# Kernel tuning notes

Measured on AMD Instinct MI355X. Metric: run time of the kernel, lower is better.

Reference implementation:

```python
import jax, jax.numpy as jnp
import numpy as np

D_MODEL = 1024
N_HEAD = 16
D_K = D_MODEL // N_HEAD
B, S = 2, 2048


def setup_inputs() -> dict:
    key = jax.random.key(0)
    ks = jax.random.split(key, 13)
    sc = 0.02
    return {
        "q": jax.random.normal(ks[0], (B, S, D_MODEL), jnp.float32),
        "k": jax.random.normal(ks[1], (B, S, D_MODEL), jnp.float32),
        "v": jax.random.normal(ks[2], (B, S, D_MODEL), jnp.float32),
        "mask": jax.random.randint(ks[3], (B, 1, S, S), 0, 2, jnp.int32),
        "Wq": jax.random.normal(ks[4], (D_MODEL, D_MODEL), jnp.float32) * sc,
        "bq": jnp.zeros((D_MODEL,), jnp.float32),
        "Wk": jax.random.normal(ks[5], (D_MODEL, D_MODEL), jnp.float32) * sc,
        "bk": jnp.zeros((D_MODEL,), jnp.float32),
        "Wv": jax.random.normal(ks[6], (D_MODEL, D_MODEL), jnp.float32) * sc,
        "bv": jnp.zeros((D_MODEL,), jnp.float32),
        "Wo": jax.random.normal(ks[7], (D_MODEL, D_MODEL), jnp.float32) * sc,
        "bo": jnp.zeros((D_MODEL,), jnp.float32),
    }


def _split_head(x):
    # (B, S, D) -> (B, H, S, d_k)
    b, s, _ = x.shape
    return x.reshape(b, s, N_HEAD, D_K).transpose(0, 2, 1, 3)


def reference(q, k, v, mask, Wq, bq, Wk, bk, Wv, bv, Wo, bo):
    qh = _split_head(q @ Wq.T + bq)
    kh = _split_head(k @ Wk.T + bk)
    vh = _split_head(v @ Wv.T + bv)
    # NOTE: original scales by sqrt(d_model), not sqrt(d_k)
    score = jnp.einsum("bhqd,bhkd->bhqk", qh, kh) / jnp.sqrt(jnp.float32(D_MODEL))
    score = jnp.where(mask == 0, jnp.float32(-1e9), score)
    attn = jax.nn.softmax(score, axis=-1)
    out = jnp.einsum("bhqk,bhkd->bhqd", attn, vh)
    out = out.transpose(0, 2, 1, 3).reshape(q.shape[0], -1, D_MODEL)
    return out @ Wo.T + bo
```

## Files before the change

kernel.cpp:

```cpp
#include <hip/hip_runtime.h>

#define D_MODEL 1024
#define N_HEAD  16
#define D_K     64
#define BATCH   2
#define SEQ     2048
#define M_ROWS  (BATCH*SEQ)
#define NT      (SEQ/64)

typedef __attribute__((ext_vector_type(8))) short short8;
typedef __attribute__((ext_vector_type(4))) float f32x4;
typedef unsigned short u16;
typedef unsigned long long u64;

#define GLDS16(g, l) \
    __builtin_amdgcn_global_load_lds((const __attribute__((address_space(1))) void*)(g), \
                                     (__attribute__((address_space(3))) void*)(l), 16, 0, 0)

#define CSC (0.03125f * 1.44269504089f)

__device__ __forceinline__ u16 f2bf(float f) {
    unsigned u = __builtin_bit_cast(unsigned, f);
    unsigned r = (u + 0x7fffu + ((u >> 16) & 1u)) >> 16;
    return (u16)r;
}

__device__ __forceinline__ float fexp2(float x) {
#if __has_builtin(__builtin_amdgcn_exp2f)
    return __builtin_amdgcn_exp2f(x);
#else
    return exp2f(x);
#endif
}

__global__ __launch_bounds__(256)
void cvt_all(const float* __restrict__ q, const float* __restrict__ k, const float* __restrict__ v,
             const float* __restrict__ wq, const float* __restrict__ wk,
             const float* __restrict__ wv, const float* __restrict__ wo,
             u16* __restrict__ qb, u16* __restrict__ kb, u16* __restrict__ vb,
             u16* __restrict__ wqb, u16* __restrict__ wkb, u16* __restrict__ wvb, u16* __restrict__ wob)
{
    const int total = 3 * 1048576 + 4 * 262144;
    int i = blockIdx.x * blockDim.x + threadIdx.x;
    const int stride = gridDim.x * blockDim.x;
    for (; i < total; i += stride) {
        const float* src; u16* dst; int loc;
        if (i < 3 * 1048576) {
            const int t = i >> 20; loc = i & 1048575;
            src = (t == 0) ? q : (t == 1) ? k : v;
            dst = (t == 0) ? qb : (t == 1) ? kb : vb;
        } else {
            const int j = i - 3 * 1048576; const int t = j >> 18; loc = j & 262143;
            src = (t == 0) ? wq : (t == 1) ? wk : (t == 2) ? wv : wo;
            dst = (t == 0) ? wqb : (t == 1) ? wkb : (t == 2) ? wvb : wob;
        }
        float4 a = ((const float4*)src)[loc];
        ushort4 o;
        o.x = f2bf(a.x); o.y = f2bf(a.y); o.z = f2bf(a.z); o.w = f2bf(a.w);
        ((ushort4*)dst)[loc] = o;
    }
}

__global__ __launch_bounds__(256)
void mask_pack(const int* __restrict__ mask, u64* __restrict__ mb, int nwords)
{
    const int lane = threadIdx.x & 63;
    int w = (blockIdx.x * blockDim.x + threadIdx.x) >> 6;
    const int nw = (gridDim.x * blockDim.x) >> 6;
    for (; w < nwords; w += nw) {
        int v = mask[(size_t)w * 64 + lane];
        u64 bits = __ballot(v != 0);
        if (lane == 0) mb[w] = bits;
    }
}

template<bool OUT_BF16, bool BIAS_ROW, bool SCALE>
__device__ __forceinline__
void gemm128_body(const u16* __restrict__ A, const u16* __restrict__ W,
                  const float* __restrict__ bias, void* __restrict__ Cout,
                  const int M, const int N, const int K, const int bx, const int by)
{
    __shared__ u16 As[2][128 * 32];
    __shared__ u16 Ws[2][128 * 32];
    const int tid = threadIdx.x, l = tid & 63, w = tid >> 6;
    const int bm = by * 128, bn = bx * 128;
    const int wr = (w >> 1) * 64, wc = (w & 1) * 64;
    const int srow = tid >> 2, scol = (tid & 3) * 8;
    const u16* Ap = A + (size_t)(bm + srow) * K + scol;
    const u16* Wp = W + (size_t)(bn + srow) * K + scol;

    f32x4 acc[4][4];
#pragma unroll
    for (int m = 0; m < 4; ++m)
#pragma unroll
        for (int n = 0; n < 4; ++n) acc[m][n] = (f32x4)0.0f;

    const int ro = l & 15, ge = (l >> 4) * 8;

    GLDS16(Ap,                  (char*)As[0] + w * 1024);
    GLDS16(Ap + (size_t)64 * K, (char*)As[0] + w * 1024 + 4096);
    GLDS16(Wp,                  (char*)Ws[0] + w * 1024);
    GLDS16(Wp + (size_t)64 * K, (char*)Ws[0] + w * 1024 + 4096);
    __syncthreads();

    int buf = 0;
    for (int k0 = 0; k0 < K; k0 += 32) {
        if (k0 + 32 < K) {
            GLDS16(Ap + k0 + 32,                  (char*)As[buf ^ 1] + w * 1024);
            GLDS16(Ap + k0 + 32 + (size_t)64 * K, (char*)As[buf ^ 1] + w * 1024 + 4096);
            GLDS16(Wp + k0 + 32,                  (char*)Ws[buf ^ 1] + w * 1024);
            GLDS16(Wp + k0 + 32 + (size_t)64 * K, (char*)Ws[buf ^ 1] + w * 1024 + 4096);
        }
        short8 a[4], b[4];
#pragma unroll
        for (int m = 0; m < 4; ++m)
            a[m] = *(const short8*)(As[buf] + (wr + m * 16 + ro) * 32 + ge);
#pragma unroll
        for (int n = 0; n < 4; ++n)
            b[n] = *(const short8*)(Ws[buf] + (wc + n * 16 + ro) * 32 + ge);
#pragma unroll
        for (int m = 0; m < 4; ++m)
#pragma unroll
            for (int n = 0; n < 4; ++n)
                acc[m][n] = __builtin_amdgcn_mfma_f32_16x16x32_bf16(a[m], b[n], acc[m][n], 0, 0, 0);
        __syncthreads();
        buf ^= 1;
    }

    const int cr = (l >> 4) * 4;
#pragma unroll
    for (int m = 0; m < 4; ++m)
#pragma unroll
        for (int n = 0; n < 4; ++n)
#pragma unroll
            for (int j = 0; j < 4; ++j) {
                const int row = bm + wr + m * 16 + cr + j;
                const int col = bn + wc + n * 16 + ro;
                float vvv = acc[m][n][j] + (BIAS_ROW ? bias[row] : bias[col]);
                if constexpr (SCALE) vvv *= CSC;
                if constexpr (OUT_BF16)
                    ((u16*)Cout)[(size_t)row * N + col] = f2bf(vvv);
                else
                    ((float*)Cout)[(size_t)row * N + col] = vvv;
            }
}

__global__ __launch_bounds__(256)
void gemm_proj(const u16* __restrict__ qb, const u16* __restrict__ kb, const u16* __restrict__ vb,
               const u16* __restrict__ wqb, const u16* __restrict__ wkb, const u16* __restrict__ wvb,
               const float* __restrict__ bq, const float* __restrict__ bk, const float* __restrict__ bv,
               u16* __restrict__ Qp, u16* __restrict__ Kp, u16* __restrict__ Vt)
{
    int lin = blockIdx.x;
    lin = (lin & 7) * 32 + (lin >> 3);
    const int z = blockIdx.y;
    if (z == 0)
        gemm128_body<true, false, true >(qb, wqb, bq, Qp, M_ROWS, D_MODEL, D_MODEL, lin & 7, lin >> 3);
    else if (z == 1)
        gemm128_body<true, false, false>(kb, wkb, bk, Kp, M_ROWS, D_MODEL, D_MODEL, lin & 7, lin >> 3);
    else
        gemm128_body<true, true,  false>(wvb, vb, bv, Vt, D_MODEL, M_ROWS, D_MODEL, lin & 31, lin >> 5);
}

__device__ __forceinline__
void gemm64_body(const u16* __restrict__ A, const u16* __restrict__ W,
                 const float* __restrict__ bias, float* __restrict__ Cout,
                 const int N, const int K, const int bx, const int by)
{
    __shared__ u16 As[2][128 * 32];
    __shared__ u16 Ws[2][64 * 32];
    const int tid = threadIdx.x, l = tid & 63, w = tid >> 6;
    const int bm = by * 128, bn = bx * 64;
    const int wr = (w >> 1) * 64, wc = (w & 1) * 32;
    const int srow = tid >> 2, scol = (tid & 3) * 8;
    const u16* Ap = A + (size_t)(bm + srow) * K + scol;
    const u16* Wp = W + (size_t)(bn + srow) * K + scol;

    f32x4 acc[4][2];
#pragma unroll
    for (int m = 0; m < 4; ++m)
#pragma unroll
        for (int n = 0; n < 2; ++n) acc[m][n] = (f32x4)0.0f;

    const int ro = l & 15, ge = (l >> 4) * 8;

    GLDS16(Ap,                  (char*)As[0] + w * 1024);
    GLDS16(Ap + (size_t)64 * K, (char*)As[0] + w * 1024 + 4096);
    GLDS16(Wp,                  (char*)Ws[0] + w * 1024);
    __syncthreads();

    int buf = 0;
    for (int k0 = 0; k0 < K; k0 += 32) {
        if (k0 + 32 < K) {
            GLDS16(Ap + k0 + 32,                  (char*)As[buf ^ 1] + w * 1024);
            GLDS16(Ap + k0 + 32 + (size_t)64 * K, (char*)As[buf ^ 1] + w * 1024 + 4096);
            GLDS16(Wp + k0 + 32,                  (char*)Ws[buf ^ 1] + w * 1024);
        }
        short8 a[4], b[2];
#pragma unroll
        for (int m = 0; m < 4; ++m)
            a[m] = *(const short8*)(As[buf] + (wr + m * 16 + ro) * 32 + ge);
#pragma unroll
        for (int n = 0; n < 2; ++n)
            b[n] = *(const short8*)(Ws[buf] + (wc + n * 16 + ro) * 32 + ge);
#pragma unroll
        for (int m = 0; m < 4; ++m)
#pragma unroll
            for (int n = 0; n < 2; ++n)
                acc[m][n] = __builtin_amdgcn_mfma_f32_16x16x32_bf16(a[m], b[n], acc[m][n], 0, 0, 0);
        __syncthreads();
        buf ^= 1;
    }

    const int cr = (l >> 4) * 4;
#pragma unroll
    for (int m = 0; m < 4; ++m)
#pragma unroll
        for (int n = 0; n < 2; ++n)
#pragma unroll
            for (int j = 0; j < 4; ++j) {
                const int row = bm + wr + m * 16 + cr + j;
                const int col = bn + wc + n * 16 + ro;
                Cout[(size_t)row * N + col] = acc[m][n][j] + bias[col];
            }
}

__global__ __launch_bounds__(256)
void gemm_out(const u16* __restrict__ Ctx, const u16* __restrict__ wob,
              const float* __restrict__ bo, float* __restrict__ out)
{
    int lin = blockIdx.y * gridDim.x + blockIdx.x;
    const int cpx = (gridDim.x * gridDim.y) >> 3;
    lin = (lin & 7) * cpx + (lin >> 3);
    const int bx = lin % gridDim.x, by = lin / gridDim.x;
    gemm64_body(Ctx, wob, bo, out, D_MODEL, D_MODEL, bx, by);
}

__global__ __launch_bounds__(256, 4)
void attn_mfma(const u16* __restrict__ Qp, const u16* __restrict__ Kp,
               const u16* __restrict__ Vt, const u64* __restrict__ mb,
               u16* __restrict__ Ctx)
{
    __shared__ char QsPs[8192];
    __shared__ char Ks[2][8192];
    __shared__ char Vs[2][8192];

    const int tid = threadIdx.x, l = tid & 63, w = tid >> 6;
    int lin = blockIdx.y * gridDim.x + blockIdx.x;
    lin = (lin & 7) * 128 + (lin >> 3);
    const int bx = lin & 31, by = lin >> 5;
    const int b = by >> 4, h = by & 15;
    const int q0 = bx * 64;
    const size_t tokbase = (size_t)b * SEQ;

    const int lrow = tid >> 3, ss = (tid & 7) ^ (lrow & 7);
    const u16* ksrc0 = Kp + (tokbase + lrow) * D_MODEL + h * 64 + ss * 8;
    const u16* vsrc0 = Vt + (size_t)(h * 64 + lrow) * M_ROWS + tokbase + ss * 8;

    {
        const u16* qsrc = Qp + (tokbase + q0 + lrow) * D_MODEL + h * 64 + ss * 8;
        GLDS16(qsrc,                          QsPs + w * 1024);
        GLDS16(qsrc + (size_t)32 * D_MODEL,   QsPs + w * 1024 + 4096);
        GLDS16(ksrc0,                         (char*)Ks[0] + w * 1024);
        GLDS16(ksrc0 + (size_t)32 * D_MODEL,  (char*)Ks[0] + w * 1024 + 4096);
        GLDS16(vsrc0,                         (char*)Vs[0] + w * 1024);
        GLDS16(vsrc0 + (size_t)32 * M_ROWS,   (char*)Vs[0] + w * 1024 + 4096);
    }
    __syncthreads();

    const int ro = l & 15, gb = (l >> 4) * 16;

    short8 qf[2];
#pragma unroll
    for (int c = 0; c < 2; ++c) {
        const int row = w * 16 + ro;
        qf[c] = *(const short8*)(QsPs + row * 128 + ((c * 64 + gb) ^ ((row & 7) << 4)));
    }

    const uint2* mptr[4];
#pragma unroll
    for (int j = 0; j < 4; ++j)
        mptr[j] = (const uint2*)(mb + (tokbase + q0 + w * 16 + (l >> 4) * 4 + j) * (size_t)NT);

    f32x4 o[4], lacc = (f32x4)0.0f;
#pragma unroll
    for (int dn = 0; dn < 4; ++dn) o[dn] = (f32x4)0.0f;

    const short8 ones = {0x3F80, 0x3F80, 0x3F80, 0x3F80, 0x3F80, 0x3F80, 0x3F80, 0x3F80};

    uint2 mw[4];
#pragma unroll
    for (int j = 0; j < 4; ++j) mw[j] = mptr[j][0];

    for (int t = 0; t < NT; ++t) {
        const int cur = t & 1;

        uint2 mc[4];
#pragma unroll
        for (int j = 0; j < 4; ++j) mc[j] = mw[j];

        if (t + 1 < NT) {
            const u16* kn = ksrc0 + (size_t)(t + 1) * 64 * D_MODEL;
            const u16* vn = vsrc0 + (t + 1) * 64;
            GLDS16(kn,                         (char*)Ks[cur ^ 1] + w * 1024);
            GLDS16(kn + (size_t)32 * D_MODEL,  (char*)Ks[cur ^ 1] + w * 1024 + 4096);
            GLDS16(vn,                         (char*)Vs[cur ^ 1] + w * 1024);
            GLDS16(vn + (size_t)32 * M_ROWS,   (char*)Vs[cur ^ 1] + w * 1024 + 4096);
#pragma unroll
            for (int j = 0; j < 4; ++j) mw[j] = mptr[j][t + 1];
        }

        f32x4 s[4];
#pragma unroll
        for (int n = 0; n < 4; ++n) {
            const int row = n * 16 + ro;
            short8 k0f = *(const short8*)(Ks[cur] + row * 128 + ((gb)      ^ ((row & 7) << 4)));
            short8 k1f = *(const short8*)(Ks[cur] + row * 128 + ((64 + gb) ^ ((row & 7) << 4)));
            f32x4 a = (f32x4)0.0f;
            a = __builtin_amdgcn_mfma_f32_16x16x32_bf16(qf[0], k0f, a, 0, 0, 0);
            a = __builtin_amdgcn_mfma_f32_16x16x32_bf16(qf[1], k1f, a, 0, 0, 0);
            s[n] = a;
        }

        char* pb = QsPs + w * 2048;
#pragma unroll
        for (int j = 0; j < 4; ++j) {
            const int prow = (l >> 4) * 4 + j;
            const int sw = (prow & 7) << 4;
            const unsigned wlo = mc[j].x >> ro;
            const unsigned whi = mc[j].y >> ro;
            float p0 = fexp2(s[0][j]); p0 = (wlo & 1u)       ? p0 : 0.f;
            float p1 = fexp2(s[1][j]); p1 = (wlo & 0x10000u) ? p1 : 0.f;
            float p2 = fexp2(s[2][j]); p2 = (whi & 1u)       ? p2 : 0.f;
            float p3 = fexp2(s[3][j]); p3 = (whi & 0x10000u) ? p3 : 0.f;
            unsigned pk01, pk23;
            asm("v_cvt_pk_bf16_f32 %0, %1, %2" : "=v"(pk01) : "v"(p0), "v"(p1));
            asm("v_cvt_pk_bf16_f32 %0, %1, %2" : "=v"(pk23) : "v"(p2), "v"(p3));
            *(u16*)(pb + prow * 128 + ((2 * (0  + ro)) ^ sw)) = (u16)pk01;
            *(u16*)(pb + prow * 128 + ((2 * (16 + ro)) ^ sw)) = (u16)(pk01 >> 16);
            *(u16*)(pb + prow * 128 + ((2 * (32 + ro)) ^ sw)) = (u16)pk23;
            *(u16*)(pb + prow * 128 + ((2 * (48 + ro)) ^ sw)) = (u16)(pk23 >> 16);
        }

        short8 pf[2];
#pragma unroll
        for (int c = 0; c < 2; ++c)
            pf[c] = *(const short8*)(pb + ro * 128 + ((c * 64 + gb) ^ ((ro & 7) << 4)));

        lacc = __builtin_amdgcn_mfma_f32_16x16x32_bf16(pf[0], ones, lacc, 0, 0, 0);
        lacc = __builtin_amdgcn_mfma_f32_16x16x32_bf16(pf[1], ones, lacc, 0, 0, 0);

#pragma unroll
        for (int dn = 0; dn < 4; ++dn) {
            const int row = dn * 16 + ro;
            short8 v0f = *(const short8*)(Vs[cur] + row * 128 + ((gb)      ^ ((row & 7) << 4)));
            short8 v1f = *(const short8*)(Vs[cur] + row * 128 + ((64 + gb) ^ ((row & 7) << 4)));
            o[dn] = __builtin_amdgcn_mfma_f32_16x16x32_bf16(pf[0], v0f, o[dn], 0, 0, 0);
            o[dn] = __builtin_amdgcn_mfma_f32_16x16x32_bf16(pf[1], v1f, o[dn], 0, 0, 0);
        }

        __syncthreads();
    }

    float inv[4];
#pragma unroll
    for (int j = 0; j < 4; ++j) inv[j] = 1.f / lacc[j];
#pragma unroll
    for (int dn = 0; dn < 4; ++dn)
#pragma unroll
        for (int j = 0; j < 4; ++j) {
            const size_t qr = tokbase + q0 + w * 16 + (l >> 4) * 4 + j;
            Ctx[qr * D_MODEL + h * 64 + dn * 16 + ro] = f2bf(o[dn][j] * inv[j]);
        }
}

extern "C" void kernel_launch(void* const* d_in, const int* in_sizes, int n_in,
                              void* d_out, int out_size, void* d_ws, size_t ws_size,
                              hipStream_t stream)
{
    const float* q    = (const float*)d_in[0];
    const float* k    = (const float*)d_in[1];
    const float* v    = (const float*)d_in[2];
    const int*   mask = (const int*)  d_in[3];
    const float* Wq   = (const float*)d_in[4];
    const float* bq   = (const float*)d_in[5];
    const float* Wk   = (const float*)d_in[6];
    const float* bk   = (const float*)d_in[7];
    const float* Wv   = (const float*)d_in[8];
    const float* bv   = (const float*)d_in[9];
    const float* Wo   = (const float*)d_in[10];
    const float* bo   = (const float*)d_in[11];
    float* out = (float*)d_out;

    u16* ws16 = (u16*)d_ws;
    const size_t M1 = 1024 * 1024;
    u16* qb  = ws16;
    u16* kb  = ws16 + 4 * M1;
    u16* vb  = ws16 + 8 * M1;
    u16* Wqb = ws16 + 12 * M1;
    u16* Wkb = ws16 + 13 * M1;
    u16* Wvb = ws16 + 14 * M1;
    u16* Wob = ws16 + 15 * M1;
    u16* Qp  = ws16 + 16 * M1;
    u16* Kp  = ws16 + 20 * M1;
    u16* Vt  = ws16 + 24 * M1;
    u16* Ctx = qb;
    u64* maskb = (u64*)vb;

    cvt_all<<<2048, 256, 0, stream>>>(q, k, v, Wq, Wk, Wv, Wo,
                                      qb, kb, vb, Wqb, Wkb, Wvb, Wob);

    dim3 gproj(256, 3);
    gemm_proj<<<gproj, 256, 0, stream>>>(qb, kb, vb, Wqb, Wkb, Wvb, bq, bk, bv, Qp, Kp, Vt);

    mask_pack<<<1024, 256, 0, stream>>>(mask, maskb, BATCH * SEQ * SEQ / 64);

    dim3 ga(SEQ / 64, BATCH * N_HEAD);
    attn_mfma<<<ga, 256, 0, stream>>>(Qp, Kp, Vt, maskb, Ctx);

    dim3 go(D_MODEL / 64, M_ROWS / 128);
    gemm_out<<<go, 256, 0, stream>>>(Ctx, Wob, bo, out);
}
```

Measured before the change: 306.1 us.

## Double attention query tile per block, permute V layout, fuse mask packing into convert

Each attention block now handles 128 query rows, with each wave owning two 16-row MFMA tiles, so every K/V tile loaded into LDS serves twice as many queries. The V projection output uses a permuted column order, which lets each lane write its P values as one 64-bit LDS store instead of four 16-bit stores. Mask packing is merged into the conversion kernel to remove a launch, and the packed mask gets its own workspace region. In exchange the attention grid is halved, register and LDS use per block rise, and the launch-bounds occupancy hint drops from 4 to 2.

```diff
diff --git a/kernel.cpp b/kernel.cpp
--- a/kernel.cpp
+++ b/kernel.cpp
@@ -34,11 +34,13 @@
 }
 
 __global__ __launch_bounds__(256)
-void cvt_all(const float* __restrict__ q, const float* __restrict__ k, const float* __restrict__ v,
-             const float* __restrict__ wq, const float* __restrict__ wk,
-             const float* __restrict__ wv, const float* __restrict__ wo,
-             u16* __restrict__ qb, u16* __restrict__ kb, u16* __restrict__ vb,
-             u16* __restrict__ wqb, u16* __restrict__ wkb, u16* __restrict__ wvb, u16* __restrict__ wob)
+void cvt_and_mask(const float* __restrict__ q, const float* __restrict__ k, const float* __restrict__ v,
+                  const float* __restrict__ wq, const float* __restrict__ wk,
+                  const float* __restrict__ wv, const float* __restrict__ wo,
+                  u16* __restrict__ qb, u16* __restrict__ kb, u16* __restrict__ vb,
+                  u16* __restrict__ wqb, u16* __restrict__ wkb, u16* __restrict__ wvb,
+                  u16* __restrict__ wob,
+                  const int* __restrict__ mask, u64* __restrict__ mb)
 {
     const int total = 3 * 1048576 + 4 * 262144;
     int i = blockIdx.x * blockDim.x + threadIdx.x;
@@ -59,22 +61,18 @@
         o.x = f2bf(a.x); o.y = f2bf(a.y); o.z = f2bf(a.z); o.w = f2bf(a.w);
         ((ushort4*)dst)[loc] = o;
     }
-}
-
-__global__ __launch_bounds__(256)
-void mask_pack(const int* __restrict__ mask, u64* __restrict__ mb, int nwords)
-{
+
     const int lane = threadIdx.x & 63;
-    int w = (blockIdx.x * blockDim.x + threadIdx.x) >> 6;
+    int wd = (blockIdx.x * blockDim.x + threadIdx.x) >> 6;
     const int nw = (gridDim.x * blockDim.x) >> 6;
-    for (; w < nwords; w += nw) {
-        int v = mask[(size_t)w * 64 + lane];
-        u64 bits = __ballot(v != 0);
-        if (lane == 0) mb[w] = bits;
-    }
-}
-
-template<bool OUT_BF16, bool BIAS_ROW, bool SCALE>
+    for (; wd < BATCH * SEQ * SEQ / 64; wd += nw) {
+        int mv = mask[(size_t)wd * 64 + lane];
+        u64 bits = __ballot(mv != 0);
+        if (lane == 0) mb[wd] = bits;
+    }
+}
+
+template<bool OUT_BF16, bool BIAS_ROW, bool SCALE, bool PERM>
 __device__ __forceinline__
 void gemm128_body(const u16* __restrict__ A, const u16* __restrict__ W,
                   const float* __restrict__ bias, void* __restrict__ Cout,
@@ -138,10 +136,12 @@
                 const int col = bn + wc + n * 16 + ro;
                 float vvv = acc[m][n][j] + (BIAS_ROW ? bias[row] : bias[col]);
                 if constexpr (SCALE) vvv *= CSC;
+                int colst = col;
+                if constexpr (PERM) colst = bn + wc + 4 * ro + n;
                 if constexpr (OUT_BF16)
-                    ((u16*)Cout)[(size_t)row * N + col] = f2bf(vvv);
+                    ((u16*)Cout)[(size_t)row * N + colst] = f2bf(vvv);
                 else
-                    ((float*)Cout)[(size_t)row * N + col] = vvv;
+                    ((float*)Cout)[(size_t)row * N + colst] = vvv;
             }
 }
 
@@ -155,11 +155,11 @@
     lin = (lin & 7) * 32 + (lin >> 3);
     const int z = blockIdx.y;
     if (z == 0)
-        gemm128_body<true, false, true >(qb, wqb, bq, Qp, M_ROWS, D_MODEL, D_MODEL, lin & 7, lin >> 3);
+        gemm128_body<true, false, true,  false>(qb, wqb, bq, Qp, M_ROWS, D_MODEL, D_MODEL, lin & 7, lin >> 3);
     else if (z == 1)
-        gemm128_body<true, false, false>(kb, wkb, bk, Kp, M_ROWS, D_MODEL, D_MODEL, lin & 7, lin >> 3);
+        gemm128_body<true, false, false, false>(kb, wkb, bk, Kp, M_ROWS, D_MODEL, D_MODEL, lin & 7, lin >> 3);
     else
-        gemm128_body<true, true,  false>(wvb, vb, bv, Vt, D_MODEL, M_ROWS, D_MODEL, lin & 31, lin >> 5);
+        gemm128_body<true, true,  false, true >(wvb, vb, bv, Vt, D_MODEL, M_ROWS, D_MODEL, lin & 31, lin >> 5);
 }
 
 __device__ __forceinline__
@@ -236,21 +236,21 @@
     gemm64_body(Ctx, wob, bo, out, D_MODEL, D_MODEL, bx, by);
 }
 
-__global__ __launch_bounds__(256, 4)
+__global__ __launch_bounds__(256, 2)
 void attn_mfma(const u16* __restrict__ Qp, const u16* __restrict__ Kp,
                const u16* __restrict__ Vt, const u64* __restrict__ mb,
                u16* __restrict__ Ctx)
 {
-    __shared__ char QsPs[8192];
+    __shared__ char QsPs[16384];
     __shared__ char Ks[2][8192];
     __shared__ char Vs[2][8192];
 
     const int tid = threadIdx.x, l = tid & 63, w = tid >> 6;
     int lin = blockIdx.y * gridDim.x + blockIdx.x;
-    lin = (lin & 7) * 128 + (lin >> 3);
-    const int bx = lin & 31, by = lin >> 5;
+    lin = (lin & 7) * 64 + (lin >> 3);
+    const int bx = lin & 15, by = lin >> 4;
     const int b = by >> 4, h = by & 15;
-    const int q0 = bx * 64;
+    const int q0 = bx * 128;
     const size_t tokbase = (size_t)b * SEQ;
 
     const int lrow = tid >> 3, ss = (tid & 7) ^ (lrow & 7);
@@ -259,45 +259,52 @@
 
     {
         const u16* qsrc = Qp + (tokbase + q0 + lrow) * D_MODEL + h * 64 + ss * 8;
-        GLDS16(qsrc,                          QsPs + w * 1024);
-        GLDS16(qsrc + (size_t)32 * D_MODEL,   QsPs + w * 1024 + 4096);
-        GLDS16(ksrc0,                         (char*)Ks[0] + w * 1024);
-        GLDS16(ksrc0 + (size_t)32 * D_MODEL,  (char*)Ks[0] + w * 1024 + 4096);
-        GLDS16(vsrc0,                         (char*)Vs[0] + w * 1024);
-        GLDS16(vsrc0 + (size_t)32 * M_ROWS,   (char*)Vs[0] + w * 1024 + 4096);
+#pragma unroll
+        for (int i = 0; i < 4; ++i)
+            GLDS16(qsrc + (size_t)32 * i * D_MODEL, QsPs + w * 1024 + i * 4096);
+        GLDS16(ksrc0,                        (char*)Ks[0] + w * 1024);
+        GLDS16(ksrc0 + (size_t)32 * D_MODEL, (char*)Ks[0] + w * 1024 + 4096);
+        GLDS16(vsrc0,                        (char*)Vs[0] + w * 1024);
+        GLDS16(vsrc0 + (size_t)32 * M_ROWS,  (char*)Vs[0] + w * 1024 + 4096);
     }
     __syncthreads();
 
-    const int ro = l & 15, gb = (l >> 4) * 16;
-
-    short8 qf[2];
-#pragma unroll
-    for (int c = 0; c < 2; ++c) {
-        const int row = w * 16 + ro;
-        qf[c] = *(const short8*)(QsPs + row * 128 + ((c * 64 + gb) ^ ((row & 7) << 4)));
-    }
-
-    const uint2* mptr[4];
-#pragma unroll
-    for (int j = 0; j < 4; ++j)
-        mptr[j] = (const uint2*)(mb + (tokbase + q0 + w * 16 + (l >> 4) * 4 + j) * (size_t)NT);
-
-    f32x4 o[4], lacc = (f32x4)0.0f;
-#pragma unroll
-    for (int dn = 0; dn < 4; ++dn) o[dn] = (f32x4)0.0f;
+    const int ro = l & 15, g = l >> 4, gb = g * 16;
+
+    short8 qf[2][2];
+#pragma unroll
+    for (int mi = 0; mi < 2; ++mi)
+#pragma unroll
+        for (int c = 0; c < 2; ++c) {
+            const int row = w * 32 + mi * 16 + ro;
+            qf[mi][c] = *(const short8*)(QsPs + row * 128 + ((c * 64 + gb) ^ ((row & 7) << 4)));
+        }
+
+    int mrow[2][4];
+#pragma unroll
+    for (int mi = 0; mi < 2; ++mi)
+#pragma unroll
+        for (int j = 0; j < 4; ++j)
+            mrow[mi][j] = (int)((tokbase + q0 + w * 32 + mi * 16 + g * 4 + j) * NT);
+
+    f32x4 o[2][4], lacc[2];
+#pragma unroll
+    for (int mi = 0; mi < 2; ++mi) {
+        lacc[mi] = (f32x4)0.0f;
+#pragma unroll
+        for (int dn = 0; dn < 4; ++dn) o[mi][dn] = (f32x4)0.0f;
+    }
 
     const short8 ones = {0x3F80, 0x3F80, 0x3F80, 0x3F80, 0x3F80, 0x3F80, 0x3F80, 0x3F80};
-
-    uint2 mw[4];
-#pragma unroll
-    for (int j = 0; j < 4; ++j) mw[j] = mptr[j][0];
 
     for (int t = 0; t < NT; ++t) {
         const int cur = t & 1;
 
-        uint2 mc[4];
-#pragma unroll
-        for (int j = 0; j < 4; ++j) mc[j] = mw[j];
+        u64 mw[2][4];
+#pragma unroll
+        for (int mi = 0; mi < 2; ++mi)
+#pragma unroll
+            for (int j = 0; j < 4; ++j) mw[mi][j] = mb[mrow[mi][j] + t];
 
         if (t + 1 < NT) {
             const u16* kn = ksrc0 + (size_t)(t + 1) * 64 * D_MODEL;
@@ -306,72 +313,89 @@
             GLDS16(kn + (size_t)32 * D_MODEL,  (char*)Ks[cur ^ 1] + w * 1024 + 4096);
             GLDS16(vn,                         (char*)Vs[cur ^ 1] + w * 1024);
             GLDS16(vn + (size_t)32 * M_ROWS,   (char*)Vs[cur ^ 1] + w * 1024 + 4096);
-#pragma unroll
-            for (int j = 0; j < 4; ++j) mw[j] = mptr[j][t + 1];
-        }
-
-        f32x4 s[4];
+        }
+
+        f32x4 s[2][4];
 #pragma unroll
         for (int n = 0; n < 4; ++n) {
             const int row = n * 16 + ro;
-            short8 k0f = *(const short8*)(Ks[cur] + row * 128 + ((gb)      ^ ((row & 7) << 4)));
-            short8 k1f = *(const short8*)(Ks[cur] + row * 128 + ((64 + gb) ^ ((row & 7) << 4)));
-            f32x4 a = (f32x4)0.0f;
-            a = __builtin_amdgcn_mfma_f32_16x16x32_bf16(qf[0], k0f, a, 0, 0, 0);
-            a = __builtin_amdgcn_mfma_f32_16x16x32_bf16(qf[1], k1f, a, 0, 0, 0);
-            s[n] = a;
-        }
-
-        char* pb = QsPs + w * 2048;
-#pragma unroll
-        for (int j = 0; j < 4; ++j) {
-            const int prow = (l >> 4) * 4 + j;
-            const int sw = (prow & 7) << 4;
-            const unsigned wlo = mc[j].x >> ro;
-            const unsigned whi = mc[j].y >> ro;
-            float p0 = fexp2(s[0][j]); p0 = (wlo & 1u)       ? p0 : 0.f;
-            float p1 = fexp2(s[1][j]); p1 = (wlo & 0x10000u) ? p1 : 0.f;
-            float p2 = fexp2(s[2][j]); p2 = (whi & 1u)       ? p2 : 0.f;
-            float p3 = fexp2(s[3][j]); p3 = (whi & 0x10000u) ? p3 : 0.f;
-            unsigned pk01, pk23;
-            asm("v_cvt_pk_bf16_f32 %0, %1, %2" : "=v"(pk01) : "v"(p0), "v"(p1));
-            asm("v_cvt_pk_bf16_f32 %0, %1, %2" : "=v"(pk23) : "v"(p2), "v"(p3));
-            *(u16*)(pb + prow * 128 + ((2 * (0  + ro)) ^ sw)) = (u16)pk01;
-            *(u16*)(pb + prow * 128 + ((2 * (16 + ro)) ^ sw)) = (u16)(pk01 >> 16);
-            *(u16*)(pb + prow * 128 + ((2 * (32 + ro)) ^ sw)) = (u16)pk23;
-            *(u16*)(pb + prow * 128 + ((2 * (48 + ro)) ^ sw)) = (u16)(pk23 >> 16);
-        }
-
-        short8 pf[2];
-#pragma unroll
-        for (int c = 0; c < 2; ++c)
-            pf[c] = *(const short8*)(pb + ro * 128 + ((c * 64 + gb) ^ ((ro & 7) << 4)));
-
-        lacc = __builtin_amdgcn_mfma_f32_16x16x32_bf16(pf[0], ones, lacc, 0, 0, 0);
-        lacc = __builtin_amdgcn_mfma_f32_16x16x32_bf16(pf[1], ones, lacc, 0, 0, 0);
+            const int sw = (row & 7) << 4;
+            short8 k0f = *(const short8*)(Ks[cur] + row * 128 + (gb ^ sw));
+            short8 k1f = *(const short8*)(Ks[cur] + row * 128 + ((64 + gb) ^ sw));
+#pragma unroll
+            for (int mi = 0; mi < 2; ++mi) {
+                f32x4 a = (f32x4)0.0f;
+                a = __builtin_amdgcn_mfma_f32_16x16x32_bf16(qf[mi][0], k0f, a, 0, 0, 0);
+                a = __builtin_amdgcn_mfma_f32_16x16x32_bf16(qf[mi][1], k1f, a, 0, 0, 0);
+                s[mi][n] = a;
+            }
+        }
+
+#pragma unroll
+        for (int mi = 0; mi < 2; ++mi) {
+            char* pb = QsPs + w * 4096 + mi * 2048;
+#pragma unroll
+            for (int j = 0; j < 4; ++j) {
+                const int prow = g * 4 + j;
+                const unsigned wlo = (unsigned)(mw[mi][j]) >> ro;
+                const unsigned whi = (unsigned)(mw[mi][j] >> 32) >> ro;
+                float p0 = fexp2(s[mi][0][j]); p0 = (wlo & 1u)       ? p0 : 0.f;
+                float p1 = fexp2(s[mi][1][j]); p1 = (wlo & 0x10000u) ? p1 : 0.f;
+                float p2 = fexp2(s[mi][2][j]); p2 = (whi & 1u)       ? p2 : 0.f;
+                float p3 = fexp2(s[mi][3][j]); p3 = (whi & 0x10000u) ? p3 : 0.f;
+                unsigned pk01, pk23;
+                asm("v_cvt_pk_bf16_f32 %0, %1, %2" : "=v"(pk01) : "v"(p0), "v"(p1));
+                asm("v_cvt_pk_bf16_f32 %0, %1, %2" : "=v"(pk23) : "v"(p2), "v"(p3));
+                const u64 pv = (u64)pk01 | ((u64)pk23 << 32);
+                *(u64*)(pb + prow * 128 + ((8 * ro) ^ ((prow & 7) << 4))) = pv;
+            }
+        }
+
+        short8 pf[2][2];
+#pragma unroll
+        for (int mi = 0; mi < 2; ++mi)
+#pragma unroll
+            for (int c = 0; c < 2; ++c) {
+                const int row = mi * 16 + ro;
+                pf[mi][c] = *(const short8*)(QsPs + w * 4096 + row * 128 +
+                                             ((c * 64 + gb) ^ ((ro & 7) << 4)));
+            }
+
+#pragma unroll
+        for (int mi = 0; mi < 2; ++mi) {
+            lacc[mi] = __builtin_amdgcn_mfma_f32_16x16x32_bf16(pf[mi][0], ones, lacc[mi], 0, 0, 0);
+            lacc[mi] = __builtin_amdgcn_mfma_f32_16x16x32_bf16(pf[mi][1], ones, lacc[mi], 0, 0, 0);
+        }
 
 #pragma unroll
         for (int dn = 0; dn < 4; ++dn) {
             const int row = dn * 16 + ro;
-            short8 v0f = *(const short8*)(Vs[cur] + row * 128 + ((gb)      ^ ((row & 7) << 4)));
-            short8 v1f = *(const short8*)(Vs[cur] + row * 128 + ((64 + gb) ^ ((row & 7) << 4)));
-            o[dn] = __builtin_amdgcn_mfma_f32_16x16x32_bf16(pf[0], v0f, o[dn], 0, 0, 0);
-            o[dn] = __builtin_amdgcn_mfma_f32_16x16x32_bf16(pf[1], v1f, o[dn], 0, 0, 0);
+            const int sw = (row & 7) << 4;
+            short8 v0f = *(const short8*)(Vs[cur] + row * 128 + (gb ^ sw));
+            short8 v1f = *(const short8*)(Vs[cur] + row * 128 + ((64 + gb) ^ sw));
+#pragma unroll
+            for (int mi = 0; mi < 2; ++mi) {
+                o[mi][dn] = __builtin_amdgcn_mfma_f32_16x16x32_bf16(pf[mi][0], v0f, o[mi][dn], 0, 0, 0);
+                o[mi][dn] = __builtin_amdgcn_mfma_f32_16x16x32_bf16(pf[mi][1], v1f, o[mi][dn], 0, 0, 0);
+            }
         }
 
         __syncthreads();
     }
 
-    float inv[4];
-#pragma unroll
-    for (int j = 0; j < 4; ++j) inv[j] = 1.f / lacc[j];
-#pragma unroll
-    for (int dn = 0; dn < 4; ++dn)
-#pragma unroll
-        for (int j = 0; j < 4; ++j) {
-            const size_t qr = tokbase + q0 + w * 16 + (l >> 4) * 4 + j;
-            Ctx[qr * D_MODEL + h * 64 + dn * 16 + ro] = f2bf(o[dn][j] * inv[j]);
-        }
+#pragma unroll
+    for (int mi = 0; mi < 2; ++mi) {
+        float inv[4];
+#pragma unroll
+        for (int j = 0; j < 4; ++j) inv[j] = 1.f / lacc[mi][j];
+#pragma unroll
+        for (int dn = 0; dn < 4; ++dn)
+#pragma unroll
+            for (int j = 0; j < 4; ++j) {
+                const size_t qr = tokbase + q0 + w * 32 + mi * 16 + g * 4 + j;
+                Ctx[qr * D_MODEL + h * 64 + dn * 16 + ro] = f2bf(o[mi][dn][j] * inv[j]);
+            }
+    }
 }
 
 extern "C" void kernel_launch(void* const* d_in, const int* in_sizes, int n_in,
@@ -404,18 +428,17 @@
     u16* Qp  = ws16 + 16 * M1;
     u16* Kp  = ws16 + 20 * M1;
     u16* Vt  = ws16 + 24 * M1;
+    u64* maskb = (u64*)(ws16 + 28 * M1);
     u16* Ctx = qb;
-    u64* maskb = (u64*)vb;
-
-    cvt_all<<<2048, 256, 0, stream>>>(q, k, v, Wq, Wk, Wv, Wo,
-                                      qb, kb, vb, Wqb, Wkb, Wvb, Wob);
+
+    cvt_and_mask<<<2048, 256, 0, stream>>>(q, k, v, Wq, Wk, Wv, Wo,
+                                           qb, kb, vb, Wqb, Wkb, Wvb, Wob,
+                                           mask, maskb);
 
     dim3 gproj(256, 3);
     gemm_proj<<<gproj, 256, 0, stream>>>(qb, kb, vb, Wqb, Wkb, Wvb, bq, bk, bv, Qp, Kp, Vt);
 
-    mask_pack<<<1024, 256, 0, stream>>>(mask, maskb, BATCH * SEQ * SEQ / 64);
-
-    dim3 ga(SEQ / 64, BATCH * N_HEAD);
+    dim3 ga(SEQ / 128, BATCH * N_HEAD);
     attn_mfma<<<ga, 256, 0, stream>>>(Qp, Kp, Vt, maskb, Ctx);
 
     dim3 go(D_MODEL / 64, M_ROWS / 128);
```

After: 295.3 us. 3.5% less time.
